# Optimization experiments

Measured on AMD Instinct MI355X. Metric: run time of the kernel, lower is better.

The kernel has to match this reference:

```python
import jax, jax.numpy as jnp
import numpy as np


def setup_inputs() -> dict:
    key = jax.random.key(0)
    k1, k2, k3 = jax.random.split(key, 3)
    B, T, F = 16, 2048, 64
    he = jax.random.normal(k1, (B, T, F), dtype=jnp.float32)
    scale = 1.0 / np.sqrt(F).astype(np.float32)
    W1 = jax.random.normal(k2, (F, F), dtype=jnp.float32) * scale
    W2 = jax.random.normal(k3, (F, F), dtype=jnp.float32) * scale
    return {"he": he, "W1": W1, "W2": W2, "attention_len": 48}


def reference(he, W1, W2, attention_len):
    # he: [B, T, F] encoder states. For each output step i the original module:
    #   1) unrolls L_i = min(attention_len, max(i,1)) decoder steps starting
    #      from he[:, i, :]:  H_k = sigmoid(H_{k-1} @ W1), Y_k = sigmoid(H_k @ W2)
    #   2) attends Y_1..Y_{L_i} against the encoder window he[:, i-L_i:i, :]
    #      with per-step dot-product scores, softmax over the window, and a
    #      weighted sum of the encoder window.
    # (i=0 degenerates to a single-element softmax -> context = he[:, 0, :].)
    B, T, F = he.shape
    A = attention_len

    def step(H, _):
        H = jax.nn.sigmoid(H @ W1)          # [B, T, F]
        Y = jax.nn.sigmoid(H @ W2)          # [B, T, F]
        return H, Y

    # Decoder outputs for every start position, all A steps: Ys[b, i, t, f]
    _, Ys = jax.lax.scan(step, he, None, length=A)   # [A, B, T, F]
    Ys = jnp.moveaxis(Ys, 0, 2)                      # [B, T, A, F]

    i = jnp.arange(T)[:, None]                       # [T, 1]
    t = jnp.arange(A)[None, :]                       # [1, A]
    L = jnp.minimum(A, jnp.maximum(i, 1))            # window length per step
    j = jnp.clip(i - L + t, 0, T - 1)                # encoder index per (i, t)
    valid = t < L                                    # [T, A]

    gathered = he[:, j, :]                           # [B, T, A, F] windowed encoder
    scores = jnp.einsum('btaf,btaf->bta', Ys, gathered)
    scores = jnp.where(valid[None, :, :], scores, jnp.float32(-1e9))
    w = jax.nn.softmax(scores, axis=-1)              # [B, T, A]
    ctx = jnp.einsum('bta,btaf->btf', w, gathered)   # [B, T, F]
    return ctx
```

## Files before the change

### kernel.cpp

```cpp
#include <hip/hip_runtime.h>

#define B_   16
#define T_   2048
#define F_   64
#define A_   48
#define TOK  64
#define WSTR 68
#define HWS  72
#define SSTR 49
#define NWIN 111

typedef __attribute__((ext_vector_type(4))) _Float16 half4;
typedef __attribute__((ext_vector_type(2))) _Float16 half2;
typedef __attribute__((ext_vector_type(4))) float    f32x4;

#define LOG2E 1.4426950408889634f

__device__ __forceinline__ float sigp(float c) {
    return __builtin_amdgcn_rcpf(1.0f + __builtin_amdgcn_exp2f(c));
}
__device__ __forceinline__ half2 pk2(float a, float b) {
    return __builtin_bit_cast(half2, __builtin_amdgcn_cvt_pkrtz(a, b));
}

struct Smem {
    float    sWin[NWIN * WSTR];
    _Float16 sWinH[NWIN * HWS];
    float    sSc[TOK * SSTR];
};

template<bool FIRST>
__device__ __forceinline__ void run_block(Smem& sm, int b, int t0,
                                          const float* __restrict__ he,
                                          const float* __restrict__ W1,
                                          const float* __restrict__ W2,
                                          float* __restrict__ out)
{
    const int tid = threadIdx.x;
    const float* __restrict__ heB = he + (size_t)b * T_ * F_;

    for (int i = tid; i < NWIN * 16; i += 256) {
        int row = i >> 4, c4 = (i & 15) * 4;
        int g = t0 - 48 + row;
        if (!FIRST || g >= 0) {
            float4 v = *(const float4*)(heB + (size_t)g * F_ + c4);
            *(float4*)(&sm.sWin[row * WSTR + c4]) = v;
            half2 lo = pk2(v.x, v.y), hi = pk2(v.z, v.w);
            half4 h; h[0] = lo[0]; h[1] = lo[1]; h[2] = hi[0]; h[3] = hi[1];
            *(half4*)(&sm.sWinH[row * HWS + c4]) = h;
        }
    }

    const int lane = tid & 63;
    const int wv   = tid >> 6;
    const int quad = lane >> 4;
    const int ml   = lane & 15;
    const int tw0  = wv * 16;
    const int tg   = t0 + tw0 + ml;
    const int L    = min(A_, max(tg, 1));

    half4 aW1[4][4], aW2[4][4];
    for (int mo = 0; mo < 4; ++mo)
        for (int kt = 0; kt < 4; ++kt) {
            half4 f1, f2;
#pragma unroll
            for (int j = 0; j < 4; ++j) {
                int k = kt * 16 + quad * 4 + j;
                f1[j] = (_Float16)(-LOG2E * W1[k * F_ + mo * 16 + ml]);
                f2[j] = (_Float16)(-LOG2E * W2[k * F_ + mo * 16 + ml]);
            }
            aW1[mo][kt] = f1; aW2[mo][kt] = f2;
        }

    half4 hb[4];
#pragma unroll
    for (int kt = 0; kt < 4; ++kt) {
        float4 v = *(const float4*)(heB + (size_t)tg * F_ + kt * 16 + quad * 4);
        half4 h;
        h[0] = (_Float16)v.x; h[1] = (_Float16)v.y;
        h[2] = (_Float16)v.z; h[3] = (_Float16)v.w;
        hb[kt] = h;
    }
    __syncthreads();

    const bool amDiag = (quad == (ml >> 2));
    const bool s0 = (ml & 3) == 0, s1 = (ml & 3) == 1, s2 = (ml & 3) == 2;
    float* scp = &sm.sSc[(tw0 + ml) * SSTR];

    const _Float16* wrow = &sm.sWinH[(tw0 + ml) * HWS + quad * 4];

#pragma unroll 4
    for (int a = 0; a < A_; ++a) {
        f32x4 c1[4];
#pragma unroll
        for (int mo = 0; mo < 4; ++mo) {
            f32x4 z = {0.f, 0.f, 0.f, 0.f};
#pragma unroll
            for (int kt = 0; kt < 4; ++kt)
                z = __builtin_amdgcn_mfma_f32_16x16x16f16(aW1[mo][kt], hb[kt], z, 0, 0, 0);
            c1[mo] = z;
        }
#pragma unroll
        for (int mo = 0; mo < 4; ++mo) {
            half2 lo = pk2(sigp(c1[mo][0]), sigp(c1[mo][1]));
            half2 hi = pk2(sigp(c1[mo][2]), sigp(c1[mo][3]));
            half4 h; h[0] = lo[0]; h[1] = lo[1]; h[2] = hi[0]; h[3] = hi[1];
            hb[mo] = h;
        }
        f32x4 c2[4];
#pragma unroll
        for (int mo = 0; mo < 4; ++mo) {
            f32x4 z = {0.f, 0.f, 0.f, 0.f};
#pragma unroll
            for (int kt = 0; kt < 4; ++kt)
                z = __builtin_amdgcn_mfma_f32_16x16x16f16(aW2[mo][kt], hb[kt], z, 0, 0, 0);
            c2[mo] = z;
        }
        half4 yh[4];
#pragma unroll
        for (int mo = 0; mo < 4; ++mo) {
            half2 lo = pk2(sigp(c2[mo][0]), sigp(c2[mo][1]));
            half2 hi = pk2(sigp(c2[mo][2]), sigp(c2[mo][3]));
            half4 h; h[0] = lo[0]; h[1] = lo[1]; h[2] = hi[0]; h[3] = hi[1];
            yh[mo] = h;
        }
        const _Float16* wp;
        if (FIRST) {
            int j = tg - L + a; if (j < 0) j = 0;
            wp = &sm.sWinH[(j + 48) * HWS + quad * 4];
        } else {
            wp = wrow; wrow += HWS;
        }
        half4 g0 = *(const half4*)(wp);
        half4 g1 = *(const half4*)(wp + 16);
        half4 g2 = *(const half4*)(wp + 32);
        half4 g3 = *(const half4*)(wp + 48);
        f32x4 zs = {0.f, 0.f, 0.f, 0.f};
        zs = __builtin_amdgcn_mfma_f32_16x16x16f16(yh[0], g0, zs, 0, 0, 0);
        zs = __builtin_amdgcn_mfma_f32_16x16x16f16(yh[1], g1, zs, 0, 0, 0);
        zs = __builtin_amdgcn_mfma_f32_16x16x16f16(yh[2], g2, zs, 0, 0, 0);
        zs = __builtin_amdgcn_mfma_f32_16x16x16f16(yh[3], g3, zs, 0, 0, 0);
        float val = s0 ? zs[0] : (s1 ? zs[1] : (s2 ? zs[2] : zs[3]));
        if (FIRST) val = (a < L) ? val : -1e9f;
        if (amDiag) scp[a] = val;
    }
    __syncthreads();

    {
        int r = tid >> 2, s = tid & 3;
        float sc[12];
#pragma unroll
        for (int i = 0; i < 12; ++i) sc[i] = sm.sSc[r * SSTR + i * 4 + s];
        float m = sc[0];
#pragma unroll
        for (int i = 1; i < 12; ++i) m = fmaxf(m, sc[i]);
        m = fmaxf(m, __shfl_xor(m, 1));
        m = fmaxf(m, __shfl_xor(m, 2));
        float e[12]; float sum = 0.f;
#pragma unroll
        for (int i = 0; i < 12; ++i) { e[i] = __expf(sc[i] - m); sum += e[i]; }
        sum += __shfl_xor(sum, 1);
        sum += __shfl_xor(sum, 2);
        float inv = __builtin_amdgcn_rcpf(sum);
#pragma unroll
        for (int i = 0; i < 12; ++i) sm.sSc[r * SSTR + i * 4 + s] = e[i] * inv;
    }
    __syncthreads();

    {
        int r = tid >> 2, fc = (tid & 3) * 16;
        int tgr = t0 + r;
        int Lr = min(A_, max(tgr, 1));
        float acc[16];
#pragma unroll
        for (int q = 0; q < 16; ++q) acc[q] = 0.f;
        for (int a = 0; a < A_; ++a) {
            float wgt = sm.sSc[r * SSTR + a];
            int j = tgr - Lr + a;
            if (FIRST) { if (j < 0) j = 0; }
            const float* wp = &sm.sWin[(j - t0 + 48) * WSTR + fc];
#pragma unroll
            for (int q = 0; q < 4; ++q) {
                float4 g = *(const float4*)(wp + q * 4);
                acc[q*4+0] += wgt * g.x; acc[q*4+1] += wgt * g.y;
                acc[q*4+2] += wgt * g.z; acc[q*4+3] += wgt * g.w;
            }
        }
        float* op = out + ((size_t)b * T_ + tgr) * F_ + fc;
#pragma unroll
        for (int q = 0; q < 4; ++q)
            *(float4*)(op + q * 4) = make_float4(acc[q*4], acc[q*4+1], acc[q*4+2], acc[q*4+3]);
    }
}

__global__ __launch_bounds__(256)
void ContextBlock_kernel(const float* __restrict__ he, const float* __restrict__ W1,
                         const float* __restrict__ W2, float* __restrict__ out)
{
    __shared__ Smem sm;
    const int blk = blockIdx.x;
    if (blk < B_ * 31) {
        int b  = blk / 31;
        int t0 = ((blk % 31) + 1) * TOK;
        run_block<false>(sm, b, t0, he, W1, W2, out);
    } else {
        int b = blk - B_ * 31;
        run_block<true>(sm, b, 0, he, W1, W2, out);
    }
}

extern "C" void kernel_launch(void* const* d_in, const int* in_sizes, int n_in,
                              void* d_out, int out_size, void* d_ws, size_t ws_size,
                              hipStream_t stream) {
    const float* he = (const float*)d_in[0];
    const float* W1 = (const float*)d_in[1];
    const float* W2 = (const float*)d_in[2];
    float* out = (float*)d_out;
    hipLaunchKernelGGL(ContextBlock_kernel, dim3(512), dim3(256), 0, stream, he, W1, W2, out);
}
```

Measured before the change: 124.3 us.

## Process two 16-token tiles per wave and drop fp32 window copy

Each block now covers 128 tokens instead of 64, so every wave carries two independent 16-token MFMA chains (A and B). The two chains interleave inside the serial 48-step recurrence to hide MFMA and sigmoid latency, and the W1/W2 register fragments are reused across twice as many tokens. The fp32 window copy in shared memory is removed, so the weighted-sum stage reads the fp16 window instead, which costs some precision in the context output. The grid is halved to 256 blocks with launch_bounds(256,1), which lowers occupancy and could leave some CUs idle on a 256-CU part.

```diff
diff --git a/kernel.cpp b/kernel.cpp
--- a/kernel.cpp
+++ b/kernel.cpp
@@ -4,13 +4,13 @@
 #define T_   2048
 #define F_   64
 #define A_   48
-#define TOK  64
-#define WSTR 68
+#define TOKB 128
 #define HWS  72
 #define SSTR 49
-#define NWIN 111
+#define NWIN 175
 
 typedef __attribute__((ext_vector_type(4))) _Float16 half4;
+typedef __attribute__((ext_vector_type(8))) _Float16 half8;
 typedef __attribute__((ext_vector_type(2))) _Float16 half2;
 typedef __attribute__((ext_vector_type(4))) float    f32x4;
 
@@ -24,9 +24,8 @@
 }
 
 struct Smem {
-    float    sWin[NWIN * WSTR];
     _Float16 sWinH[NWIN * HWS];
-    float    sSc[TOK * SSTR];
+    float    sSc[TOKB * SSTR];
 };
 
 template<bool FIRST>
@@ -44,7 +43,6 @@
         int g = t0 - 48 + row;
         if (!FIRST || g >= 0) {
             float4 v = *(const float4*)(heB + (size_t)g * F_ + c4);
-            *(float4*)(&sm.sWin[row * WSTR + c4]) = v;
             half2 lo = pk2(v.x, v.y), hi = pk2(v.z, v.w);
             half4 h; h[0] = lo[0]; h[1] = lo[1]; h[2] = hi[0]; h[3] = hi[1];
             *(half4*)(&sm.sWinH[row * HWS + c4]) = h;
@@ -55,9 +53,11 @@
     const int wv   = tid >> 6;
     const int quad = lane >> 4;
     const int ml   = lane & 15;
-    const int tw0  = wv * 16;
-    const int tg   = t0 + tw0 + ml;
-    const int L    = min(A_, max(tg, 1));
+    const int base = wv * 32;
+    const int tgA  = t0 + base + ml;
+    const int tgB  = tgA + 16;
+    const int LA   = min(A_, max(tgA, 1));
+    const int LB   = min(A_, max(tgB, 1));
 
     half4 aW1[4][4], aW2[4][4];
     for (int mo = 0; mo < 4; ++mo)
@@ -72,139 +72,172 @@
             aW1[mo][kt] = f1; aW2[mo][kt] = f2;
         }
 
-    half4 hb[4];
+    half4 hbA[4], hbB[4];
 #pragma unroll
     for (int kt = 0; kt < 4; ++kt) {
-        float4 v = *(const float4*)(heB + (size_t)tg * F_ + kt * 16 + quad * 4);
-        half4 h;
-        h[0] = (_Float16)v.x; h[1] = (_Float16)v.y;
-        h[2] = (_Float16)v.z; h[3] = (_Float16)v.w;
-        hb[kt] = h;
+        float4 vA = *(const float4*)(heB + (size_t)tgA * F_ + kt * 16 + quad * 4);
+        float4 vB = *(const float4*)(heB + (size_t)tgB * F_ + kt * 16 + quad * 4);
+        half4 hA, hB;
+        hA[0] = (_Float16)vA.x; hA[1] = (_Float16)vA.y;
+        hA[2] = (_Float16)vA.z; hA[3] = (_Float16)vA.w;
+        hB[0] = (_Float16)vB.x; hB[1] = (_Float16)vB.y;
+        hB[2] = (_Float16)vB.z; hB[3] = (_Float16)vB.w;
+        hbA[kt] = hA; hbB[kt] = hB;
     }
     __syncthreads();
 
     const bool amDiag = (quad == (ml >> 2));
     const bool s0 = (ml & 3) == 0, s1 = (ml & 3) == 1, s2 = (ml & 3) == 2;
-    float* scp = &sm.sSc[(tw0 + ml) * SSTR];
-
-    const _Float16* wrow = &sm.sWinH[(tw0 + ml) * HWS + quad * 4];
-
-#pragma unroll 4
+    float* scpA = &sm.sSc[(base + ml) * SSTR];
+    float* scpB = scpA + 16 * SSTR;
+
+    const _Float16* wrowA = &sm.sWinH[(base + ml) * HWS + quad * 4];
+    const _Float16* wrowB = wrowA + 16 * HWS;
+
+#pragma unroll 2
     for (int a = 0; a < A_; ++a) {
-        f32x4 c1[4];
+        const _Float16 *wpA, *wpB;
+        if (FIRST) {
+            int jA = tgA - LA + a; if (jA < 0) jA = 0;
+            int jB = tgB - LB + a; if (jB < 0) jB = 0;
+            wpA = &sm.sWinH[(jA + 48) * HWS + quad * 4];
+            wpB = &sm.sWinH[(jB + 48) * HWS + quad * 4];
+        } else {
+            wpA = wrowA; wrowA += HWS;
+            wpB = wrowB; wrowB += HWS;
+        }
+        half4 gA0 = *(const half4*)(wpA);      half4 gB0 = *(const half4*)(wpB);
+        half4 gA1 = *(const half4*)(wpA + 16); half4 gB1 = *(const half4*)(wpB + 16);
+        half4 gA2 = *(const half4*)(wpA + 32); half4 gB2 = *(const half4*)(wpB + 32);
+        half4 gA3 = *(const half4*)(wpA + 48); half4 gB3 = *(const half4*)(wpB + 48);
+
+        f32x4 c1A[4], c1B[4];
 #pragma unroll
         for (int mo = 0; mo < 4; ++mo) {
-            f32x4 z = {0.f, 0.f, 0.f, 0.f};
-#pragma unroll
-            for (int kt = 0; kt < 4; ++kt)
-                z = __builtin_amdgcn_mfma_f32_16x16x16f16(aW1[mo][kt], hb[kt], z, 0, 0, 0);
-            c1[mo] = z;
+            f32x4 zA = {0.f, 0.f, 0.f, 0.f}, zB = {0.f, 0.f, 0.f, 0.f};
+#pragma unroll
+            for (int kt = 0; kt < 4; ++kt) {
+                zA = __builtin_amdgcn_mfma_f32_16x16x16f16(aW1[mo][kt], hbA[kt], zA, 0, 0, 0);
+                zB = __builtin_amdgcn_mfma_f32_16x16x16f16(aW1[mo][kt], hbB[kt], zB, 0, 0, 0);
+            }
+            c1A[mo] = zA; c1B[mo] = zB;
         }
 #pragma unroll
         for (int mo = 0; mo < 4; ++mo) {
-            half2 lo = pk2(sigp(c1[mo][0]), sigp(c1[mo][1]));
-            half2 hi = pk2(sigp(c1[mo][2]), sigp(c1[mo][3]));
-            half4 h; h[0] = lo[0]; h[1] = lo[1]; h[2] = hi[0]; h[3] = hi[1];
-            hb[mo] = h;
-        }
-        f32x4 c2[4];
+            half2 loA = pk2(sigp(c1A[mo][0]), sigp(c1A[mo][1]));
+            half2 hiA = pk2(sigp(c1A[mo][2]), sigp(c1A[mo][3]));
+            half2 loB = pk2(sigp(c1B[mo][0]), sigp(c1B[mo][1]));
+            half2 hiB = pk2(sigp(c1B[mo][2]), sigp(c1B[mo][3]));
+            half4 hA; hA[0] = loA[0]; hA[1] = loA[1]; hA[2] = hiA[0]; hA[3] = hiA[1];
+            half4 hB; hB[0] = loB[0]; hB[1] = loB[1]; hB[2] = hiB[0]; hB[3] = hiB[1];
+            hbA[mo] = hA; hbB[mo] = hB;
+        }
+        f32x4 c2A[4], c2B[4];
 #pragma unroll
         for (int mo = 0; mo < 4; ++mo) {
-            f32x4 z = {0.f, 0.f, 0.f, 0.f};
-#pragma unroll
-            for (int kt = 0; kt < 4; ++kt)
-                z = __builtin_amdgcn_mfma_f32_16x16x16f16(aW2[mo][kt], hb[kt], z, 0, 0, 0);
-            c2[mo] = z;
-        }
-        half4 yh[4];
-#pragma unroll
-        for (int mo = 0; mo < 4; ++mo) {
-            half2 lo = pk2(sigp(c2[mo][0]), sigp(c2[mo][1]));
-            half2 hi = pk2(sigp(c2[mo][2]), sigp(c2[mo][3]));
-            half4 h; h[0] = lo[0]; h[1] = lo[1]; h[2] = hi[0]; h[3] = hi[1];
-            yh[mo] = h;
-        }
-        const _Float16* wp;
+            f32x4 zA = {0.f, 0.f, 0.f, 0.f}, zB = {0.f, 0.f, 0.f, 0.f};
+#pragma unroll
+            for (int kt = 0; kt < 4; ++kt) {
+                zA = __builtin_amdgcn_mfma_f32_16x16x16f16(aW2[mo][kt], hbA[kt], zA, 0, 0, 0);
+                zB = __builtin_amdgcn_mfma_f32_16x16x16f16(aW2[mo][kt], hbB[kt], zB, 0, 0, 0);
+            }
+            c2A[mo] = zA; c2B[mo] = zB;
+        }
+        f32x4 zsA = {0.f, 0.f, 0.f, 0.f}, zsB = {0.f, 0.f, 0.f, 0.f};
+        {
+            half4 yA[4], yB[4];
+#pragma unroll
+            for (int mo = 0; mo < 4; ++mo) {
+                half2 loA = pk2(sigp(c2A[mo][0]), sigp(c2A[mo][1]));
+                half2 hiA = pk2(sigp(c2A[mo][2]), sigp(c2A[mo][3]));
+                half2 loB = pk2(sigp(c2B[mo][0]), sigp(c2B[mo][1]));
+                half2 hiB = pk2(sigp(c2B[mo][2]), sigp(c2B[mo][3]));
+                half4 hA; hA[0] = loA[0]; hA[1] = loA[1]; hA[2] = hiA[0]; hA[3] = hiA[1];
+                half4 hB; hB[0] = loB[0]; hB[1] = loB[1]; hB[2] = hiB[0]; hB[3] = hiB[1];
+                yA[mo] = hA; yB[mo] = hB;
+            }
+            zsA = __builtin_amdgcn_mfma_f32_16x16x16f16(yA[0], gA0, zsA, 0, 0, 0);
+            zsB = __builtin_amdgcn_mfma_f32_16x16x16f16(yB[0], gB0, zsB, 0, 0, 0);
+            zsA = __builtin_amdgcn_mfma_f32_16x16x16f16(yA[1], gA1, zsA, 0, 0, 0);
+            zsB = __builtin_amdgcn_mfma_f32_16x16x16f16(yB[1], gB1, zsB, 0, 0, 0);
+            zsA = __builtin_amdgcn_mfma_f32_16x16x16f16(yA[2], gA2, zsA, 0, 0, 0);
+            zsB = __builtin_amdgcn_mfma_f32_16x16x16f16(yB[2], gB2, zsB, 0, 0, 0);
+            zsA = __builtin_amdgcn_mfma_f32_16x16x16f16(yA[3], gA3, zsA, 0, 0, 0);
+            zsB = __builtin_amdgcn_mfma_f32_16x16x16f16(yB[3], gB3, zsB, 0, 0, 0);
+        }
+        float vA = s0 ? zsA[0] : (s1 ? zsA[1] : (s2 ? zsA[2] : zsA[3]));
+        float vB = s0 ? zsB[0] : (s1 ? zsB[1] : (s2 ? zsB[2] : zsB[3]));
         if (FIRST) {
-            int j = tg - L + a; if (j < 0) j = 0;
-            wp = &sm.sWinH[(j + 48) * HWS + quad * 4];
-        } else {
-            wp = wrow; wrow += HWS;
-        }
-        half4 g0 = *(const half4*)(wp);
-        half4 g1 = *(const half4*)(wp + 16);
-        half4 g2 = *(const half4*)(wp + 32);
-        half4 g3 = *(const half4*)(wp + 48);
-        f32x4 zs = {0.f, 0.f, 0.f, 0.f};
-        zs = __builtin_amdgcn_mfma_f32_16x16x16f16(yh[0], g0, zs, 0, 0, 0);
-        zs = __builtin_amdgcn_mfma_f32_16x16x16f16(yh[1], g1, zs, 0, 0, 0);
-        zs = __builtin_amdgcn_mfma_f32_16x16x16f16(yh[2], g2, zs, 0, 0, 0);
-        zs = __builtin_amdgcn_mfma_f32_16x16x16f16(yh[3], g3, zs, 0, 0, 0);
-        float val = s0 ? zs[0] : (s1 ? zs[1] : (s2 ? zs[2] : zs[3]));
-        if (FIRST) val = (a < L) ? val : -1e9f;
-        if (amDiag) scp[a] = val;
+            vA = (a < LA) ? vA : -1e9f;
+            vB = (a < LB) ? vB : -1e9f;
+        }
+        if (amDiag) { scpA[a] = vA; scpB[a] = vB; }
     }
     __syncthreads();
 
     {
-        int r = tid >> 2, s = tid & 3;
-        float sc[12];
-#pragma unroll
-        for (int i = 0; i < 12; ++i) sc[i] = sm.sSc[r * SSTR + i * 4 + s];
+        int r = tid >> 1, s = tid & 1;
+        float sc[24];
+#pragma unroll
+        for (int i = 0; i < 24; ++i) sc[i] = sm.sSc[r * SSTR + i * 2 + s];
         float m = sc[0];
 #pragma unroll
-        for (int i = 1; i < 12; ++i) m = fmaxf(m, sc[i]);
+        for (int i = 1; i < 24; ++i) m = fmaxf(m, sc[i]);
         m = fmaxf(m, __shfl_xor(m, 1));
-        m = fmaxf(m, __shfl_xor(m, 2));
-        float e[12]; float sum = 0.f;
-#pragma unroll
-        for (int i = 0; i < 12; ++i) { e[i] = __expf(sc[i] - m); sum += e[i]; }
+        float e[24]; float sum = 0.f;
+#pragma unroll
+        for (int i = 0; i < 24; ++i) { e[i] = __expf(sc[i] - m); sum += e[i]; }
         sum += __shfl_xor(sum, 1);
-        sum += __shfl_xor(sum, 2);
         float inv = __builtin_amdgcn_rcpf(sum);
 #pragma unroll
-        for (int i = 0; i < 12; ++i) sm.sSc[r * SSTR + i * 4 + s] = e[i] * inv;
+        for (int i = 0; i < 24; ++i) sm.sSc[r * SSTR + i * 2 + s] = e[i] * inv;
     }
     __syncthreads();
 
     {
-        int r = tid >> 2, fc = (tid & 3) * 16;
+        int r = tid >> 1, fc = (tid & 1) * 32;
         int tgr = t0 + r;
         int Lr = min(A_, max(tgr, 1));
-        float acc[16];
-#pragma unroll
-        for (int q = 0; q < 16; ++q) acc[q] = 0.f;
+        float acc[32];
+#pragma unroll
+        for (int q = 0; q < 32; ++q) acc[q] = 0.f;
         for (int a = 0; a < A_; ++a) {
             float wgt = sm.sSc[r * SSTR + a];
-            int j = tgr - Lr + a;
-            if (FIRST) { if (j < 0) j = 0; }
-            const float* wp = &sm.sWin[(j - t0 + 48) * WSTR + fc];
+            int row;
+            if (FIRST) {
+                int j = tgr - Lr + a; if (j < 0) j = 0;
+                row = j + 48;
+            } else {
+                row = r + a;
+            }
+            const _Float16* wp = &sm.sWinH[row * HWS + fc];
 #pragma unroll
             for (int q = 0; q < 4; ++q) {
-                float4 g = *(const float4*)(wp + q * 4);
-                acc[q*4+0] += wgt * g.x; acc[q*4+1] += wgt * g.y;
-                acc[q*4+2] += wgt * g.z; acc[q*4+3] += wgt * g.w;
+                half8 h = *(const half8*)(wp + q * 8);
+#pragma unroll
+                for (int u = 0; u < 8; ++u)
+                    acc[q * 8 + u] += wgt * (float)h[u];
             }
         }
         float* op = out + ((size_t)b * T_ + tgr) * F_ + fc;
 #pragma unroll
-        for (int q = 0; q < 4; ++q)
+        for (int q = 0; q < 8; ++q)
             *(float4*)(op + q * 4) = make_float4(acc[q*4], acc[q*4+1], acc[q*4+2], acc[q*4+3]);
     }
 }
 
-__global__ __launch_bounds__(256)
+__global__ __launch_bounds__(256, 1)
 void ContextBlock_kernel(const float* __restrict__ he, const float* __restrict__ W1,
                          const float* __restrict__ W2, float* __restrict__ out)
 {
     __shared__ Smem sm;
     const int blk = blockIdx.x;
-    if (blk < B_ * 31) {
-        int b  = blk / 31;
-        int t0 = ((blk % 31) + 1) * TOK;
+    if (blk < B_ * 15) {
+        int b  = blk / 15;
+        int t0 = ((blk % 15) + 1) * TOKB;
         run_block<false>(sm, b, t0, he, W1, W2, out);
     } else {
-        int b = blk - B_ * 31;
+        int b = blk - B_ * 15;
         run_block<true>(sm, b, 0, he, W1, W2, out);
     }
 }
@@ -216,5 +249,5 @@
     const float* W1 = (const float*)d_in[1];
     const float* W2 = (const float*)d_in[2];
     float* out = (float*)d_out;
-    hipLaunchKernelGGL(ContextBlock_kernel, dim3(512), dim3(256), 0, stream, he, W1, W2, out);
-}
+    hipLaunchKernelGGL(ContextBlock_kernel, dim3(256), dim3(256), 0, stream, he, W1, W2, out);
+}
```

Measured after the change: 127.4 us. 1.02x slower.

## Software-pipeline decoder recurrence and drop fp32 window copy from shared memory

Applied to the files above, without the earlier changes.

Restructures the per-step loop so the score MFMAs for step a-1 are issued alongside the W1 GEMM for step a, letting independent MFMA chains overlap the dependent sigmoid recurrence. Removes the fp32 encoder window from shared memory and computes the weighted context sum from the fp16 copy, which shrinks LDS use (allowing more resident blocks) and halves the LDS read traffic in that phase. Also uses packed conversion helpers for the fp16 casts. The trade is reduced precision in the context accumulation inputs, since it now reads fp16 rather than fp32 encoder values.

```diff
diff --git a/kernel.cpp b/kernel.cpp
--- a/kernel.cpp
+++ b/kernel.cpp
@@ -5,13 +5,12 @@
 #define F_   64
 #define A_   48
 #define TOK  64
-#define WSTR 68
 #define HWS  72
 #define SSTR 49
 #define NWIN 111
 
 typedef __attribute__((ext_vector_type(4))) _Float16 half4;
-typedef __attribute__((ext_vector_type(2))) _Float16 half2;
+typedef __attribute__((ext_vector_type(8))) _Float16 half8;
 typedef __attribute__((ext_vector_type(4))) float    f32x4;
 
 #define LOG2E 1.4426950408889634f
@@ -19,12 +18,14 @@
 __device__ __forceinline__ float sigp(float c) {
     return __builtin_amdgcn_rcpf(1.0f + __builtin_amdgcn_exp2f(c));
 }
-__device__ __forceinline__ half2 pk2(float a, float b) {
-    return __builtin_bit_cast(half2, __builtin_amdgcn_cvt_pkrtz(a, b));
+__device__ __forceinline__ half4 mk4(float a, float b, float c, float d) {
+    unsigned lo = __builtin_bit_cast(unsigned, __builtin_amdgcn_cvt_pkrtz(a, b));
+    unsigned hi = __builtin_bit_cast(unsigned, __builtin_amdgcn_cvt_pkrtz(c, d));
+    uint2 u = make_uint2(lo, hi);
+    return __builtin_bit_cast(half4, u);
 }
 
 struct Smem {
-    float    sWin[NWIN * WSTR];
     _Float16 sWinH[NWIN * HWS];
     float    sSc[TOK * SSTR];
 };
@@ -44,10 +45,7 @@
         int g = t0 - 48 + row;
         if (!FIRST || g >= 0) {
             float4 v = *(const float4*)(heB + (size_t)g * F_ + c4);
-            *(float4*)(&sm.sWin[row * WSTR + c4]) = v;
-            half2 lo = pk2(v.x, v.y), hi = pk2(v.z, v.w);
-            half4 h; h[0] = lo[0]; h[1] = lo[1]; h[2] = hi[0]; h[3] = hi[1];
-            *(half4*)(&sm.sWinH[row * HWS + c4]) = h;
+            *(half4*)(&sm.sWinH[row * HWS + c4]) = mk4(v.x, v.y, v.z, v.w);
         }
     }
 
@@ -76,74 +74,66 @@
 #pragma unroll
     for (int kt = 0; kt < 4; ++kt) {
         float4 v = *(const float4*)(heB + (size_t)tg * F_ + kt * 16 + quad * 4);
-        half4 h;
-        h[0] = (_Float16)v.x; h[1] = (_Float16)v.y;
-        h[2] = (_Float16)v.z; h[3] = (_Float16)v.w;
-        hb[kt] = h;
+        hb[kt] = mk4(v.x, v.y, v.z, v.w);
     }
     __syncthreads();
 
     const bool amDiag = (quad == (ml >> 2));
     const bool s0 = (ml & 3) == 0, s1 = (ml & 3) == 1, s2 = (ml & 3) == 2;
     float* scp = &sm.sSc[(tw0 + ml) * SSTR];
-
-    const _Float16* wrow = &sm.sWinH[(tw0 + ml) * HWS + quad * 4];
-
-#pragma unroll 4
-    for (int a = 0; a < A_; ++a) {
-        f32x4 c1[4];
+    const f32x4 kZero = {0.f, 0.f, 0.f, 0.f};
+
+    auto gemm = [&](const half4 (&aW)[4][4], const half4 (&hv)[4], f32x4 (&co)[4]) {
 #pragma unroll
         for (int mo = 0; mo < 4; ++mo) {
-            f32x4 z = {0.f, 0.f, 0.f, 0.f};
-#pragma unroll
-            for (int kt = 0; kt < 4; ++kt)
-                z = __builtin_amdgcn_mfma_f32_16x16x16f16(aW1[mo][kt], hb[kt], z, 0, 0, 0);
-            c1[mo] = z;
-        }
-#pragma unroll
-        for (int mo = 0; mo < 4; ++mo) {
-            half2 lo = pk2(sigp(c1[mo][0]), sigp(c1[mo][1]));
-            half2 hi = pk2(sigp(c1[mo][2]), sigp(c1[mo][3]));
-            half4 h; h[0] = lo[0]; h[1] = lo[1]; h[2] = hi[0]; h[3] = hi[1];
-            hb[mo] = h;
-        }
-        f32x4 c2[4];
-#pragma unroll
-        for (int mo = 0; mo < 4; ++mo) {
-            f32x4 z = {0.f, 0.f, 0.f, 0.f};
-#pragma unroll
-            for (int kt = 0; kt < 4; ++kt)
-                z = __builtin_amdgcn_mfma_f32_16x16x16f16(aW2[mo][kt], hb[kt], z, 0, 0, 0);
-            c2[mo] = z;
-        }
-        half4 yh[4];
-#pragma unroll
-        for (int mo = 0; mo < 4; ++mo) {
-            half2 lo = pk2(sigp(c2[mo][0]), sigp(c2[mo][1]));
-            half2 hi = pk2(sigp(c2[mo][2]), sigp(c2[mo][3]));
-            half4 h; h[0] = lo[0]; h[1] = lo[1]; h[2] = hi[0]; h[3] = hi[1];
-            yh[mo] = h;
-        }
+            f32x4 z = __builtin_amdgcn_mfma_f32_16x16x16f16(aW[mo][0], hv[0], kZero, 0, 0, 0);
+#pragma unroll
+            for (int kt = 1; kt < 4; ++kt)
+                z = __builtin_amdgcn_mfma_f32_16x16x16f16(aW[mo][kt], hv[kt], z, 0, 0, 0);
+            co[mo] = z;
+        }
+    };
+    auto do_score = [&](int s, const f32x4 (&c2)[4]) {
+        half4 y0 = mk4(sigp(c2[0][0]), sigp(c2[0][1]), sigp(c2[0][2]), sigp(c2[0][3]));
+        half4 y1 = mk4(sigp(c2[1][0]), sigp(c2[1][1]), sigp(c2[1][2]), sigp(c2[1][3]));
+        half4 y2 = mk4(sigp(c2[2][0]), sigp(c2[2][1]), sigp(c2[2][2]), sigp(c2[2][3]));
+        half4 y3 = mk4(sigp(c2[3][0]), sigp(c2[3][1]), sigp(c2[3][2]), sigp(c2[3][3]));
         const _Float16* wp;
         if (FIRST) {
-            int j = tg - L + a; if (j < 0) j = 0;
+            int j = tg - L + s; if (j < 0) j = 0;
             wp = &sm.sWinH[(j + 48) * HWS + quad * 4];
         } else {
-            wp = wrow; wrow += HWS;
+            wp = &sm.sWinH[(tw0 + ml + s) * HWS + quad * 4];
         }
         half4 g0 = *(const half4*)(wp);
         half4 g1 = *(const half4*)(wp + 16);
         half4 g2 = *(const half4*)(wp + 32);
         half4 g3 = *(const half4*)(wp + 48);
-        f32x4 zs = {0.f, 0.f, 0.f, 0.f};
-        zs = __builtin_amdgcn_mfma_f32_16x16x16f16(yh[0], g0, zs, 0, 0, 0);
-        zs = __builtin_amdgcn_mfma_f32_16x16x16f16(yh[1], g1, zs, 0, 0, 0);
-        zs = __builtin_amdgcn_mfma_f32_16x16x16f16(yh[2], g2, zs, 0, 0, 0);
-        zs = __builtin_amdgcn_mfma_f32_16x16x16f16(yh[3], g3, zs, 0, 0, 0);
-        float val = s0 ? zs[0] : (s1 ? zs[1] : (s2 ? zs[2] : zs[3]));
-        if (FIRST) val = (a < L) ? val : -1e9f;
-        if (amDiag) scp[a] = val;
-    }
+        f32x4 zs = __builtin_amdgcn_mfma_f32_16x16x16f16(y0, g0, kZero, 0, 0, 0);
+        zs = __builtin_amdgcn_mfma_f32_16x16x16f16(y1, g1, zs, 0, 0, 0);
+        zs = __builtin_amdgcn_mfma_f32_16x16x16f16(y2, g2, zs, 0, 0, 0);
+        zs = __builtin_amdgcn_mfma_f32_16x16x16f16(y3, g3, zs, 0, 0, 0);
+        float v = s0 ? zs[0] : (s1 ? zs[1] : (s2 ? zs[2] : zs[3]));
+        if (FIRST) v = (s < L) ? v : -1e9f;
+        if (amDiag) scp[s] = v;
+    };
+
+    f32x4 c1[4], c2p[4];
+    gemm(aW1, hb, c1);
+#pragma unroll
+    for (int mo = 0; mo < 4; ++mo)
+        hb[mo] = mk4(sigp(c1[mo][0]), sigp(c1[mo][1]), sigp(c1[mo][2]), sigp(c1[mo][3]));
+    gemm(aW2, hb, c2p);
+#pragma unroll 2
+    for (int a = 1; a < A_; ++a) {
+        gemm(aW1, hb, c1);
+        do_score(a - 1, c2p);
+#pragma unroll
+        for (int mo = 0; mo < 4; ++mo)
+            hb[mo] = mk4(sigp(c1[mo][0]), sigp(c1[mo][1]), sigp(c1[mo][2]), sigp(c1[mo][3]));
+        gemm(aW2, hb, c2p);
+    }
+    do_score(A_ - 1, c2p);
     __syncthreads();
 
     {
@@ -176,14 +166,20 @@
         for (int q = 0; q < 16; ++q) acc[q] = 0.f;
         for (int a = 0; a < A_; ++a) {
             float wgt = sm.sSc[r * SSTR + a];
-            int j = tgr - Lr + a;
-            if (FIRST) { if (j < 0) j = 0; }
-            const float* wp = &sm.sWin[(j - t0 + 48) * WSTR + fc];
-#pragma unroll
-            for (int q = 0; q < 4; ++q) {
-                float4 g = *(const float4*)(wp + q * 4);
-                acc[q*4+0] += wgt * g.x; acc[q*4+1] += wgt * g.y;
-                acc[q*4+2] += wgt * g.z; acc[q*4+3] += wgt * g.w;
+            int row;
+            if (FIRST) {
+                int j = tgr - Lr + a; if (j < 0) j = 0;
+                row = j + 48;
+            } else {
+                row = r + a;
+            }
+            const _Float16* wp = &sm.sWinH[row * HWS + fc];
+#pragma unroll
+            for (int q = 0; q < 2; ++q) {
+                half8 h = *(const half8*)(wp + q * 8);
+#pragma unroll
+                for (int u = 0; u < 8; ++u)
+                    acc[q * 8 + u] += wgt * (float)h[u];
             }
         }
         float* op = out + ((size_t)b * T_ + tgr) * F_ + fc;
```

Result: slower. 130.7 us (+5.1%).
